# Kernel optimization log

Hardware: AMD Instinct MI355X
Metric: run time of the kernel (lower is better)

The kernel has to match this reference:

```python
import jax, jax.numpy as jnp
import numpy as np

N_NODES = 100000
N_EDGES = 3200000
IN_F, HID, OUT_F = 128, 3, 4


def setup_inputs() -> dict:
    key = jax.random.key(0)
    k1, k2, k3, k4, k5, k6 = jax.random.split(key, 6)
    x = jax.random.normal(k1, (N_NODES, IN_F), dtype=jnp.float32)
    edge_index = jax.random.randint(k2, (2, N_EDGES), 0, N_NODES, dtype=jnp.int64)
    # GCNConv weight (glorot) + bias, Linear(3,4) weight + bias
    W = jax.random.normal(k3, (IN_F, HID), dtype=jnp.float32) * (1.0 / np.sqrt(IN_F))
    b = jnp.zeros((HID,), dtype=jnp.float32)
    Wout = jax.random.normal(k4, (HID, OUT_F), dtype=jnp.float32) * (1.0 / np.sqrt(HID))
    bout = jax.random.normal(k5, (OUT_F,), dtype=jnp.float32) * 0.01
    return {"x": x, "edge_index": edge_index, "W": W, "b": b, "Wout": Wout, "bout": bout}


def reference(x, edge_index, W, b, Wout, bout):
    N = x.shape[0]
    # add self loops (PyG GCNConv default: add_self_loops=True)
    loop = jnp.arange(N, dtype=edge_index.dtype)
    row = jnp.concatenate([edge_index[0], loop])  # source nodes
    col = jnp.concatenate([edge_index[1], loop])  # destination nodes
    # linear transform first (cheaper: 128 -> 3)
    xw = x @ W  # [N, 3]
    # symmetric degree normalization: deg computed on destination index
    deg = jax.ops.segment_sum(jnp.ones_like(col, dtype=x.dtype), col, num_segments=N)
    dinv = jnp.where(deg > 0, jax.lax.rsqrt(deg), 0.0)
    norm = dinv[row] * dinv[col]  # [E+N]
    # gather source features, scale, scatter-add to destinations
    msg = xw[row] * norm[:, None]  # [E+N, 3]
    agg = jax.ops.segment_sum(msg, col, num_segments=N)  # [N, 3]
    h = jax.nn.relu(agg + b)
    z = h @ Wout + bout
    return (h, z)
```

## Files before the change

kernel.cpp:

```cpp
#include <hip/hip_runtime.h>
#include <hip/hip_fp16.h>

#define N_NODES 100000
#define N_EDGES 3200000
#define IN_F    128
#define HID     3
#define OUT_F   4

#define DSH     10
#define DTILE   1024
#define DMASK   1023
#define NSTRIPE 98
#define SSH     12
#define STILE   4096
#define SMASK   4095
#define NTILE   25
#define NCH     16

#define NBLKA   1024
#define THRA    256
#define EPB     ((N_EDGES + NBLKA - 1) / NBLKA)
#define N1      (NSTRIPE * NBLKA)

#define SCAN_ITEMS 16
#define SCAN_BLOCK 256
#define SCAN_PER_BLOCK (SCAN_ITEMS * SCAN_BLOCK)
#define NS1 ((N1 + SCAN_PER_BLOCK - 1) / SCAN_PER_BLOCK)

#define PSZ (NSTRIPE * DTILE * 3)

typedef float f32x4 __attribute__((ext_vector_type(4)));

__global__ void xw_kernel(const float* __restrict__ x,
                          const float* __restrict__ W,
                          float* __restrict__ xw) {
    int wave = threadIdx.x >> 6;
    int lane = threadIdx.x & 63;
    int half = lane >> 5;
    int l    = lane & 31;
    int node = blockIdx.x * 8 + wave * 2 + half;
    if (node >= N_NODES) return;
    f32x4 xv = __builtin_nontemporal_load(
        reinterpret_cast<const f32x4*>(x + (size_t)node * IN_F + l * 4));
    const float* w = W + l * 4 * HID;
    float s0 = xv.x * w[0] + xv.y * w[3] + xv.z * w[6] + xv.w * w[9];
    float s1 = xv.x * w[1] + xv.y * w[4] + xv.z * w[7] + xv.w * w[10];
    float s2 = xv.x * w[2] + xv.y * w[5] + xv.z * w[8] + xv.w * w[11];
    #pragma unroll
    for (int off = 16; off > 0; off >>= 1) {
        s0 += __shfl_down(s0, off, 32);
        s1 += __shfl_down(s1, off, 32);
        s2 += __shfl_down(s2, off, 32);
    }
    if (l == 0) {
        xw[node * 3 + 0] = s0;
        xw[node * 3 + 1] = s1;
        xw[node * 3 + 2] = s2;
    }
}

__global__ __launch_bounds__(THRA) void hist1_kernel(const int* __restrict__ col,
                                                     int* __restrict__ histG) {
    __shared__ int hist[8 * NSTRIPE];
    int tid = threadIdx.x, blk = blockIdx.x;
    for (int i = tid; i < 8 * NSTRIPE; i += THRA) hist[i] = 0;
    __syncthreads();
    int start = blk * EPB, end = min(start + EPB, N_EDGES);
    for (int e = start + tid; e < end; e += THRA)
        atomicAdd(&hist[(tid & 7) * NSTRIPE +
                        (__builtin_nontemporal_load(&col[e]) >> DSH)], 1);
    __syncthreads();
    for (int s = tid; s < NSTRIPE; s += THRA) {
        int v = 0;
        #pragma unroll
        for (int r = 0; r < 8; ++r) v += hist[r * NSTRIPE + s];
        histG[s * NBLKA + blk] = v;
    }
}

__global__ void scan1_kernel(int* __restrict__ data, int* __restrict__ bsum) {
    __shared__ int s[SCAN_BLOCK];
    int tid = threadIdx.x;
    int base = blockIdx.x * SCAN_PER_BLOCK + tid * SCAN_ITEMS;
    int v[SCAN_ITEMS];
    int tsum = 0;
    #pragma unroll
    for (int j = 0; j < SCAN_ITEMS; ++j) {
        v[j] = (base + j < N1) ? data[base + j] : 0;
        tsum += v[j];
    }
    s[tid] = tsum;
    __syncthreads();
    for (int off = 1; off < SCAN_BLOCK; off <<= 1) {
        int t = (tid >= off) ? s[tid - off] : 0;
        __syncthreads();
        s[tid] += t;
        __syncthreads();
    }
    int run = s[tid] - tsum;
    #pragma unroll
    for (int j = 0; j < SCAN_ITEMS; ++j) {
        int t = v[j];
        if (base + j < N1) data[base + j] = run;
        run += t;
    }
    if (tid == SCAN_BLOCK - 1) bsum[blockIdx.x] = s[SCAN_BLOCK - 1];
}

__global__ void scan2_kernel(int* __restrict__ bsum) {
    __shared__ int s[SCAN_BLOCK];
    int tid = threadIdx.x;
    int v = (tid < NS1) ? bsum[tid] : 0;
    s[tid] = v;
    __syncthreads();
    for (int off = 1; off < SCAN_BLOCK; off <<= 1) {
        int t = (tid >= off) ? s[tid - off] : 0;
        __syncthreads();
        s[tid] += t;
        __syncthreads();
    }
    if (tid < NS1) bsum[tid] = s[tid] - v;
}

__global__ void scan3_kernel(int* __restrict__ data, const int* __restrict__ bsum) {
    int i = blockIdx.x * blockDim.x + threadIdx.x;
    if (i < N1) data[i] += bsum[i / SCAN_PER_BLOCK];
}

__global__ __launch_bounds__(THRA) void fill1_kernel(const int* __restrict__ row,
                                                     const int* __restrict__ col,
                                                     const int* __restrict__ histG,
                                                     int* __restrict__ packed1) {
    __shared__ int offs[NSTRIPE];
    int tid = threadIdx.x, blk = blockIdx.x;
    for (int i = tid; i < NSTRIPE; i += THRA) offs[i] = histG[i * NBLKA + blk];
    __syncthreads();
    int start = blk * EPB, end = min(start + EPB, N_EDGES);
    for (int e = start + tid; e < end; e += THRA) {
        int c = __builtin_nontemporal_load(&col[e]);
        int r = __builtin_nontemporal_load(&row[e]);
        int s = c >> DSH;
        int pos = atomicAdd(&offs[s], 1);
        packed1[pos] = (r << DSH) | (c & DMASK);
    }
}

__global__ __launch_bounds__(1024) void prep_kernel(const int* __restrict__ histG,
                                                    const int* __restrict__ packed1,
                                                    const float* __restrict__ xw,
                                                    uint2* __restrict__ tab,
                                                    int* __restrict__ off2) {
    __shared__ int cnt[DTILE];
    __shared__ int h2[NTILE * NCH];
    __shared__ int sc[NTILE * NCH];
    int tid = threadIdx.x, s = blockIdx.x;
    for (int i = tid; i < DTILE; i += 1024) cnt[i] = 0;
    if (tid < NTILE * NCH) h2[tid] = 0;
    __syncthreads();
    int seg0 = histG[s * NBLKA];
    int seg1 = (s + 1 < NSTRIPE) ? histG[(s + 1) * NBLKA] : N_EDGES;
    int seglen = seg1 - seg0;
    int chsz = (seglen + NCH - 1) / NCH;
    if (chsz == 0) chsz = 1;
    for (int i = seg0 + tid; i < seg1; i += 1024) {
        int p = __builtin_nontemporal_load(&packed1[i]);
        atomicAdd(&cnt[p & DMASK], 1);
        int t = p >> (DSH + SSH);
        int ch = (i - seg0) / chsz;
        atomicAdd(&h2[t * NCH + ch], 1);
    }
    __syncthreads();
    if (tid < NTILE * NCH) sc[tid] = h2[tid];
    __syncthreads();
    for (int off = 1; off < NTILE * NCH; off <<= 1) {
        int v = 0;
        if (tid < NTILE * NCH && tid >= off) v = sc[tid - off];
        __syncthreads();
        if (tid < NTILE * NCH) sc[tid] += v;
        __syncthreads();
    }
    if (tid < NTILE * NCH)
        off2[s * (NTILE * NCH) + tid] = seg0 + sc[tid] - h2[tid];
    if (tid < DTILE) {
        int node = s * DTILE + tid;
        if (node < N_NODES) {
            float d = rsqrtf((float)(cnt[tid] + 1));
            __half2 lo = __floats2half2_rn(xw[node * 3 + 0] * d, xw[node * 3 + 1] * d);
            __half2 hi = __floats2half2_rn(xw[node * 3 + 2] * d, d);
            uint2 u;
            u.x = *reinterpret_cast<unsigned int*>(&lo);
            u.y = *reinterpret_cast<unsigned int*>(&hi);
            tab[node] = u;
        }
    }
}

__global__ __launch_bounds__(256) void fill2_kernel(const int* __restrict__ histG,
                                                    const int* __restrict__ off2,
                                                    const int* __restrict__ packed1,
                                                    int* __restrict__ packed2) {
    __shared__ int offs[NTILE];
    int tid = threadIdx.x;
    int s = blockIdx.x >> 4;
    int c = blockIdx.x & (NCH - 1);
    int seg0 = histG[s * NBLKA];
    int seg1 = (s + 1 < NSTRIPE) ? histG[(s + 1) * NBLKA] : N_EDGES;
    int seglen = seg1 - seg0;
    int chsz = (seglen + NCH - 1) / NCH;
    if (chsz == 0) chsz = 1;
    if (tid < NTILE) offs[tid] = off2[s * (NTILE * NCH) + tid * NCH + c];
    __syncthreads();
    int lo = seg0 + c * chsz;
    int hi = min(lo + chsz, seg1);
    for (int i = lo + tid; i < hi; i += 256) {
        int p = __builtin_nontemporal_load(&packed1[i]);
        int t = p >> (DSH + SSH);
        int pos = atomicAdd(&offs[t], 1);
        packed2[pos] = (((p >> DSH) & SMASK) << DSH) | (p & DMASK);
    }
}

__global__ __launch_bounds__(512) void aggF_kernel(const int* __restrict__ histG,
                                                   const int* __restrict__ off2,
                                                   const int* __restrict__ packed2,
                                                   const uint2* __restrict__ tab,
                                                   float* __restrict__ partial) {
    __shared__ uint2 stab[STILE];
    __shared__ float acc[DTILE * 3];
    const int tq[5] = {0, 7, 13, 19, 25};
    int tid = threadIdx.x;
    int s = blockIdx.x >> 2;
    int q = blockIdx.x & 3;
    for (int i = tid; i < DTILE * 3; i += 512) acc[i] = 0.f;
    int seg1 = (s + 1 < NSTRIPE) ? histG[(s + 1) * NBLKA] : N_EDGES;
    for (int t = tq[q]; t < tq[q + 1]; ++t) {
        __syncthreads();
        for (int i = tid; i < STILE; i += 512) {
            int g = t * STILE + i;
            uint2 u = (g < N_NODES) ? tab[g] : make_uint2(0u, 0u);
            stab[i] = u;
        }
        __syncthreads();
        int b0 = off2[s * (NTILE * NCH) + t * NCH];
        int b1 = (t + 1 < NTILE) ? off2[s * (NTILE * NCH) + (t + 1) * NCH] : seg1;
        for (int i = b0 + tid; i < b1; i += 512) {
            int p = __builtin_nontemporal_load(&packed2[i]);
            uint2 v = stab[p >> DSH];
            __half2 lo = *reinterpret_cast<__half2*>(&v.x);
            __half2 hi = *reinterpret_cast<__half2*>(&v.y);
            float2 f0 = __half22float2(lo);
            float2 f1 = __half22float2(hi);
            int a = (p & DMASK) * 3;
            atomicAdd(&acc[a + 0], f0.x);
            atomicAdd(&acc[a + 1], f0.y);
            atomicAdd(&acc[a + 2], f1.x);
        }
    }
    __syncthreads();
    float* P = partial + (size_t)q * PSZ + (size_t)s * (DTILE * 3);
    for (int i = tid; i < DTILE * 3; i += 512) P[i] = acc[i];
}

__global__ __launch_bounds__(256) void final_kernel(const float* __restrict__ partial,
                                                    const uint2* __restrict__ tab,
                                                    const float* __restrict__ bb,
                                                    const float* __restrict__ Wout,
                                                    const float* __restrict__ bout,
                                                    float* __restrict__ out) {
    int i = blockIdx.x * 256 + threadIdx.x;
    if (i >= N_NODES) return;
    uint2 u = tab[i];
    __half2 lo = *reinterpret_cast<__half2*>(&u.x);
    __half2 hi = *reinterpret_cast<__half2*>(&u.y);
    float2 f0 = __half22float2(lo);
    float2 f1 = __half22float2(hi);
    float g0 = f0.x, g1 = f0.y, g2 = f1.x;
    float di = f1.y;
    #pragma unroll
    for (int q = 0; q < 4; ++q) {
        const float* P = partial + (size_t)q * PSZ + (size_t)i * 3;
        g0 += P[0];
        g1 += P[1];
        g2 += P[2];
    }
    float h0 = fmaxf(g0 * di + bb[0], 0.f);
    float h1 = fmaxf(g1 * di + bb[1], 0.f);
    float h2 = fmaxf(g2 * di + bb[2], 0.f);
    out[i * 3 + 0] = h0;
    out[i * 3 + 1] = h1;
    out[i * 3 + 2] = h2;
    float* z = out + (size_t)N_NODES * 3;
    #pragma unroll
    for (int k = 0; k < 4; ++k) {
        z[i * 4 + k] = bout[k] + h0 * Wout[0 * 4 + k] + h1 * Wout[1 * 4 + k]
                                 + h2 * Wout[2 * 4 + k];
    }
}

static inline size_t align256(size_t x) { return (x + 255) & ~(size_t)255; }

extern "C" void kernel_launch(void* const* d_in, const int* in_sizes, int n_in,
                              void* d_out, int out_size, void* d_ws, size_t ws_size,
                              hipStream_t stream) {
    const float* x    = (const float*)d_in[0];
    const int*   ei   = (const int*)d_in[1];
    const float* W    = (const float*)d_in[2];
    const float* b    = (const float*)d_in[3];
    const float* Wout = (const float*)d_in[4];
    const float* bout = (const float*)d_in[5];
    float* out = (float*)d_out;

    char* wsb = (char*)d_ws;
    size_t off = 0;
    int*   histG   = (int*)(wsb + off);  off = align256(off + (size_t)N1 * 4);
    int*   packed1 = (int*)(wsb + off);  off = align256(off + (size_t)N_EDGES * 4);
    int*   packed2 = (int*)(wsb + off);  off = align256(off + (size_t)N_EDGES * 4);
    float* xw      = (float*)(wsb + off); off = align256(off + (size_t)N_NODES * 3 * 4);
    uint2* tab     = (uint2*)(wsb + off); off = align256(off + (size_t)N_NODES * 8);
    int*   off2    = (int*)(wsb + off);  off = align256(off + (size_t)NSTRIPE * NTILE * NCH * 4);
    float* partial = (float*)(wsb + off); off = align256(off + (size_t)4 * PSZ * 4);
    int*   bsum    = (int*)(wsb + off);  off = align256(off + (size_t)NS1 * 4);

    const int* row = ei;
    const int* col = ei + N_EDGES;

    xw_kernel<<<(N_NODES + 7) / 8, 256, 0, stream>>>(x, W, xw);
    hist1_kernel<<<NBLKA, THRA, 0, stream>>>(col, histG);
    scan1_kernel<<<NS1, SCAN_BLOCK, 0, stream>>>(histG, bsum);
    scan2_kernel<<<1, SCAN_BLOCK, 0, stream>>>(bsum);
    scan3_kernel<<<(N1 + 255) / 256, 256, 0, stream>>>(histG, bsum);
    fill1_kernel<<<NBLKA, THRA, 0, stream>>>(row, col, histG, packed1);
    prep_kernel<<<NSTRIPE, 1024, 0, stream>>>(histG, packed1, xw, tab, off2);
    fill2_kernel<<<NSTRIPE * NCH, 256, 0, stream>>>(histG, off2, packed1, packed2);
    aggF_kernel<<<NSTRIPE * 4, 512, 0, stream>>>(histG, off2, packed2, tab, partial);
    final_kernel<<<(N_NODES + 255) / 256, 256, 0, stream>>>(partial, tab, b, Wout, bout, out);
}
```

Baseline: 282.4 us.

## Replace two-level bucketing with per-stripe LDS radix sort and CSR gather-reduce

Shrinks destination stripes to 256 nodes and radix-sorts each stripe's packed edges in shared memory by local destination id, producing CSR offsets and sorted source lists. A new gather kernel sums source features per destination with four threads each and fuses ReLU and the output linear layer. This removes the second fill pass, the LDS float atomics, the 4-way partial buffers and the final combine kernel. It risks silently dropping edges if a stripe exceeds the fixed shared-memory capacity, and the sort's heavy LDS use limits occupancy.

```diff
diff --git a/kernel.cpp b/kernel.cpp
--- a/kernel.cpp
+++ b/kernel.cpp
@@ -7,15 +7,12 @@
 #define HID     3
 #define OUT_F   4
 
-#define DSH     10
-#define DTILE   1024
-#define DMASK   1023
-#define NSTRIPE 98
-#define SSH     12
-#define STILE   4096
-#define SMASK   4095
-#define NTILE   25
-#define NCH     16
+#define DBITS   8
+#define DTILE   256
+#define DMASK   255
+#define NSTRIPE 391
+#define MAXE    12288
+#define MAXIT   24
 
 #define NBLKA   1024
 #define THRA    256
@@ -26,8 +23,6 @@
 #define SCAN_BLOCK 256
 #define SCAN_PER_BLOCK (SCAN_ITEMS * SCAN_BLOCK)
 #define NS1 ((N1 + SCAN_PER_BLOCK - 1) / SCAN_PER_BLOCK)
-
-#define PSZ (NSTRIPE * DTILE * 3)
 
 typedef float f32x4 __attribute__((ext_vector_type(4)));
 
@@ -68,7 +63,7 @@
     int start = blk * EPB, end = min(start + EPB, N_EDGES);
     for (int e = start + tid; e < end; e += THRA)
         atomicAdd(&hist[(tid & 7) * NSTRIPE +
-                        (__builtin_nontemporal_load(&col[e]) >> DSH)], 1);
+                        (__builtin_nontemporal_load(&col[e]) >> DBITS)], 1);
     __syncthreads();
     for (int s = tid; s < NSTRIPE; s += THRA) {
         int v = 0;
@@ -139,161 +134,166 @@
     for (int e = start + tid; e < end; e += THRA) {
         int c = __builtin_nontemporal_load(&col[e]);
         int r = __builtin_nontemporal_load(&row[e]);
-        int s = c >> DSH;
+        int s = c >> DBITS;
         int pos = atomicAdd(&offs[s], 1);
-        packed1[pos] = (r << DSH) | (c & DMASK);
-    }
-}
-
-__global__ __launch_bounds__(1024) void prep_kernel(const int* __restrict__ histG,
-                                                    const int* __restrict__ packed1,
-                                                    const float* __restrict__ xw,
-                                                    uint2* __restrict__ tab,
-                                                    int* __restrict__ off2) {
-    __shared__ int cnt[DTILE];
-    __shared__ int h2[NTILE * NCH];
-    __shared__ int sc[NTILE * NCH];
+        packed1[pos] = (r << DBITS) | (c & DMASK);
+    }
+}
+
+__global__ __launch_bounds__(512, 1) void sortA_kernel(const int* __restrict__ histG,
+                                                       const int* __restrict__ packed1,
+                                                       const float* __restrict__ xw,
+                                                       uint2* __restrict__ tab,
+                                                       int* __restrict__ csrOff,
+                                                       int* __restrict__ srcSorted) {
+    __shared__ int ping[MAXE];
+    __shared__ int pong[MAXE];
+    __shared__ int cntW[4 * MAXIT * 8];
+    __shared__ int bounds[DTILE + 1];
     int tid = threadIdx.x, s = blockIdx.x;
-    for (int i = tid; i < DTILE; i += 1024) cnt[i] = 0;
-    if (tid < NTILE * NCH) h2[tid] = 0;
-    __syncthreads();
+    int lane = tid & 63, wv = tid >> 6;
+    unsigned long long ltmask = (lane == 63) ? ~0ULL >> 1
+                                             : (1ULL << lane) - 1;
+
     int seg0 = histG[s * NBLKA];
     int seg1 = (s + 1 < NSTRIPE) ? histG[(s + 1) * NBLKA] : N_EDGES;
-    int seglen = seg1 - seg0;
-    int chsz = (seglen + NCH - 1) / NCH;
-    if (chsz == 0) chsz = 1;
-    for (int i = seg0 + tid; i < seg1; i += 1024) {
-        int p = __builtin_nontemporal_load(&packed1[i]);
-        atomicAdd(&cnt[p & DMASK], 1);
-        int t = p >> (DSH + SSH);
-        int ch = (i - seg0) / chsz;
-        atomicAdd(&h2[t * NCH + ch], 1);
-    }
-    __syncthreads();
-    if (tid < NTILE * NCH) sc[tid] = h2[tid];
-    __syncthreads();
-    for (int off = 1; off < NTILE * NCH; off <<= 1) {
-        int v = 0;
-        if (tid < NTILE * NCH && tid >= off) v = sc[tid - off];
-        __syncthreads();
-        if (tid < NTILE * NCH) sc[tid] += v;
-        __syncthreads();
-    }
-    if (tid < NTILE * NCH)
-        off2[s * (NTILE * NCH) + tid] = seg0 + sc[tid] - h2[tid];
+    int len = min(seg1 - seg0, MAXE);
+    int nIter = (len + 511) >> 9;
+
+    for (int i = tid; i < len; i += 512)
+        ping[i] = __builtin_nontemporal_load(&packed1[seg0 + i]);
+    __syncthreads();
+
+    int* srcb = ping;
+    int* dstb = pong;
+    for (int shift = 0; shift < DBITS; shift += 2) {
+        for (int it = 0; it < nIter; ++it) {
+            int idx = it * 512 + tid;
+            int bk = (idx < len) ? ((srcb[idx] >> shift) & 3) : -1;
+            unsigned long long m0 = __ballot(bk == 0);
+            unsigned long long m1 = __ballot(bk == 1);
+            unsigned long long m2 = __ballot(bk == 2);
+            unsigned long long m3 = __ballot(bk == 3);
+            if (lane == 0) {
+                cntW[(0 * nIter + it) * 8 + wv] = __popcll(m0);
+                cntW[(1 * nIter + it) * 8 + wv] = __popcll(m1);
+                cntW[(2 * nIter + it) * 8 + wv] = __popcll(m2);
+                cntW[(3 * nIter + it) * 8 + wv] = __popcll(m3);
+            }
+        }
+        __syncthreads();
+        if (wv == 0) {
+            int n = 4 * nIter * 8;
+            int carry = 0;
+            int nch = (n + 63) >> 6;
+            for (int c = 0; c < nch; ++c) {
+                int i = c * 64 + lane;
+                int v = (i < n) ? cntW[i] : 0;
+                int x = v;
+                #pragma unroll
+                for (int o = 1; o < 64; o <<= 1) {
+                    int t = __shfl_up(x, o, 64);
+                    if (lane >= o) x += t;
+                }
+                if (i < n) cntW[i] = carry + x - v;
+                carry += __shfl(x, 63, 64);
+            }
+        }
+        __syncthreads();
+        for (int it = 0; it < nIter; ++it) {
+            int idx = it * 512 + tid;
+            int p = (idx < len) ? srcb[idx] : 0;
+            int bk = (idx < len) ? ((p >> shift) & 3) : -1;
+            unsigned long long m0 = __ballot(bk == 0);
+            unsigned long long m1 = __ballot(bk == 1);
+            unsigned long long m2 = __ballot(bk == 2);
+            unsigned long long m3 = __ballot(bk == 3);
+            if (idx < len) {
+                unsigned long long mk = (bk == 0) ? m0 : (bk == 1) ? m1
+                                      : (bk == 2) ? m2 : m3;
+                int base = cntW[(bk * nIter + it) * 8 + wv];
+                int rank = __popcll(mk & ltmask);
+                dstb[base + rank] = p;
+            }
+        }
+        __syncthreads();
+        int* t = srcb; srcb = dstb; dstb = t;
+    }
+    if (tid <= DTILE) {
+        int target = tid;
+        int lo = 0, hi = len;
+        while (lo < hi) {
+            int mid = (lo + hi) >> 1;
+            if ((ping[mid] & DMASK) < target) lo = mid + 1; else hi = mid;
+        }
+        bounds[tid] = lo;
+    }
+    __syncthreads();
+    int nodeBase = s * DTILE;
+    if (tid <= DTILE) {
+        int node = nodeBase + tid;
+        if (node <= N_NODES) csrOff[node] = seg0 + bounds[tid];
+    }
     if (tid < DTILE) {
-        int node = s * DTILE + tid;
+        int node = nodeBase + tid;
         if (node < N_NODES) {
-            float d = rsqrtf((float)(cnt[tid] + 1));
-            __half2 lo = __floats2half2_rn(xw[node * 3 + 0] * d, xw[node * 3 + 1] * d);
-            __half2 hi = __floats2half2_rn(xw[node * 3 + 2] * d, d);
+            int deg = bounds[tid + 1] - bounds[tid];
+            float d = rsqrtf((float)(deg + 1));
+            __half2 lo2 = __floats2half2_rn(xw[node * 3 + 0] * d, xw[node * 3 + 1] * d);
+            __half2 hi2 = __floats2half2_rn(xw[node * 3 + 2] * d, d);
             uint2 u;
-            u.x = *reinterpret_cast<unsigned int*>(&lo);
-            u.y = *reinterpret_cast<unsigned int*>(&hi);
+            u.x = *reinterpret_cast<unsigned int*>(&lo2);
+            u.y = *reinterpret_cast<unsigned int*>(&hi2);
             tab[node] = u;
         }
     }
-}
-
-__global__ __launch_bounds__(256) void fill2_kernel(const int* __restrict__ histG,
-                                                    const int* __restrict__ off2,
-                                                    const int* __restrict__ packed1,
-                                                    int* __restrict__ packed2) {
-    __shared__ int offs[NTILE];
-    int tid = threadIdx.x;
-    int s = blockIdx.x >> 4;
-    int c = blockIdx.x & (NCH - 1);
-    int seg0 = histG[s * NBLKA];
-    int seg1 = (s + 1 < NSTRIPE) ? histG[(s + 1) * NBLKA] : N_EDGES;
-    int seglen = seg1 - seg0;
-    int chsz = (seglen + NCH - 1) / NCH;
-    if (chsz == 0) chsz = 1;
-    if (tid < NTILE) offs[tid] = off2[s * (NTILE * NCH) + tid * NCH + c];
-    __syncthreads();
-    int lo = seg0 + c * chsz;
-    int hi = min(lo + chsz, seg1);
-    for (int i = lo + tid; i < hi; i += 256) {
-        int p = __builtin_nontemporal_load(&packed1[i]);
-        int t = p >> (DSH + SSH);
-        int pos = atomicAdd(&offs[t], 1);
-        packed2[pos] = (((p >> DSH) & SMASK) << DSH) | (p & DMASK);
-    }
-}
-
-__global__ __launch_bounds__(512) void aggF_kernel(const int* __restrict__ histG,
-                                                   const int* __restrict__ off2,
-                                                   const int* __restrict__ packed2,
-                                                   const uint2* __restrict__ tab,
-                                                   float* __restrict__ partial) {
-    __shared__ uint2 stab[STILE];
-    __shared__ float acc[DTILE * 3];
-    const int tq[5] = {0, 7, 13, 19, 25};
-    int tid = threadIdx.x;
-    int s = blockIdx.x >> 2;
-    int q = blockIdx.x & 3;
-    for (int i = tid; i < DTILE * 3; i += 512) acc[i] = 0.f;
-    int seg1 = (s + 1 < NSTRIPE) ? histG[(s + 1) * NBLKA] : N_EDGES;
-    for (int t = tq[q]; t < tq[q + 1]; ++t) {
-        __syncthreads();
-        for (int i = tid; i < STILE; i += 512) {
-            int g = t * STILE + i;
-            uint2 u = (g < N_NODES) ? tab[g] : make_uint2(0u, 0u);
-            stab[i] = u;
-        }
-        __syncthreads();
-        int b0 = off2[s * (NTILE * NCH) + t * NCH];
-        int b1 = (t + 1 < NTILE) ? off2[s * (NTILE * NCH) + (t + 1) * NCH] : seg1;
-        for (int i = b0 + tid; i < b1; i += 512) {
-            int p = __builtin_nontemporal_load(&packed2[i]);
-            uint2 v = stab[p >> DSH];
-            __half2 lo = *reinterpret_cast<__half2*>(&v.x);
-            __half2 hi = *reinterpret_cast<__half2*>(&v.y);
-            float2 f0 = __half22float2(lo);
-            float2 f1 = __half22float2(hi);
-            int a = (p & DMASK) * 3;
-            atomicAdd(&acc[a + 0], f0.x);
-            atomicAdd(&acc[a + 1], f0.y);
-            atomicAdd(&acc[a + 2], f1.x);
-        }
-    }
-    __syncthreads();
-    float* P = partial + (size_t)q * PSZ + (size_t)s * (DTILE * 3);
-    for (int i = tid; i < DTILE * 3; i += 512) P[i] = acc[i];
-}
-
-__global__ __launch_bounds__(256) void final_kernel(const float* __restrict__ partial,
-                                                    const uint2* __restrict__ tab,
-                                                    const float* __restrict__ bb,
-                                                    const float* __restrict__ Wout,
-                                                    const float* __restrict__ bout,
-                                                    float* __restrict__ out) {
-    int i = blockIdx.x * 256 + threadIdx.x;
-    if (i >= N_NODES) return;
-    uint2 u = tab[i];
-    __half2 lo = *reinterpret_cast<__half2*>(&u.x);
-    __half2 hi = *reinterpret_cast<__half2*>(&u.y);
-    float2 f0 = __half22float2(lo);
-    float2 f1 = __half22float2(hi);
-    float g0 = f0.x, g1 = f0.y, g2 = f1.x;
-    float di = f1.y;
-    #pragma unroll
-    for (int q = 0; q < 4; ++q) {
-        const float* P = partial + (size_t)q * PSZ + (size_t)i * 3;
-        g0 += P[0];
-        g1 += P[1];
-        g2 += P[2];
-    }
-    float h0 = fmaxf(g0 * di + bb[0], 0.f);
-    float h1 = fmaxf(g1 * di + bb[1], 0.f);
-    float h2 = fmaxf(g2 * di + bb[2], 0.f);
-    out[i * 3 + 0] = h0;
-    out[i * 3 + 1] = h1;
-    out[i * 3 + 2] = h2;
-    float* z = out + (size_t)N_NODES * 3;
-    #pragma unroll
-    for (int k = 0; k < 4; ++k) {
-        z[i * 4 + k] = bout[k] + h0 * Wout[0 * 4 + k] + h1 * Wout[1 * 4 + k]
-                                 + h2 * Wout[2 * 4 + k];
+    for (int i = tid; i < len; i += 512)
+        srcSorted[seg0 + i] = ping[i] >> DBITS;
+}
+
+__global__ __launch_bounds__(512) void reduceB_kernel(const int* __restrict__ csrOff,
+                                                      const int* __restrict__ srcSorted,
+                                                      const uint2* __restrict__ tab,
+                                                      const float* __restrict__ bb,
+                                                      const float* __restrict__ Wout,
+                                                      const float* __restrict__ bout,
+                                                      float* __restrict__ out) {
+    int gid = blockIdx.x * 512 + threadIdx.x;
+    int dest = gid >> 2, sub = gid & 3;
+    if (dest >= N_NODES) return;
+    int start = csrOff[dest], end = csrOff[dest + 1];
+    float a0 = 0.f, a1 = 0.f, a2 = 0.f;
+    for (int i = start + sub; i < end; i += 4) {
+        int r = srcSorted[i];
+        uint2 u = tab[r];
+        __half2 lo = *reinterpret_cast<__half2*>(&u.x);
+        __half2 hi = *reinterpret_cast<__half2*>(&u.y);
+        float2 f0 = __half22float2(lo);
+        float2 f1 = __half22float2(hi);
+        a0 += f0.x; a1 += f0.y; a2 += f1.x;
+    }
+    a0 += __shfl_down(a0, 2, 64); a1 += __shfl_down(a1, 2, 64); a2 += __shfl_down(a2, 2, 64);
+    a0 += __shfl_down(a0, 1, 64); a1 += __shfl_down(a1, 1, 64); a2 += __shfl_down(a2, 1, 64);
+    if (sub == 0) {
+        uint2 u = tab[dest];
+        __half2 lo = *reinterpret_cast<__half2*>(&u.x);
+        __half2 hi = *reinterpret_cast<__half2*>(&u.y);
+        float2 f0 = __half22float2(lo);
+        float2 f1 = __half22float2(hi);
+        float di = f1.y;
+        float h0 = fmaxf((a0 + f0.x) * di + bb[0], 0.f);
+        float h1 = fmaxf((a1 + f0.y) * di + bb[1], 0.f);
+        float h2 = fmaxf((a2 + f1.x) * di + bb[2], 0.f);
+        out[dest * 3 + 0] = h0;
+        out[dest * 3 + 1] = h1;
+        out[dest * 3 + 2] = h2;
+        float* z = out + (size_t)N_NODES * 3;
+        #pragma unroll
+        for (int k = 0; k < 4; ++k) {
+            z[dest * 4 + k] = bout[k] + h0 * Wout[0 * 4 + k]
+                                      + h1 * Wout[1 * 4 + k]
+                                      + h2 * Wout[2 * 4 + k];
+        }
     }
 }
 
@@ -312,14 +312,13 @@
 
     char* wsb = (char*)d_ws;
     size_t off = 0;
-    int*   histG   = (int*)(wsb + off);  off = align256(off + (size_t)N1 * 4);
-    int*   packed1 = (int*)(wsb + off);  off = align256(off + (size_t)N_EDGES * 4);
-    int*   packed2 = (int*)(wsb + off);  off = align256(off + (size_t)N_EDGES * 4);
-    float* xw      = (float*)(wsb + off); off = align256(off + (size_t)N_NODES * 3 * 4);
-    uint2* tab     = (uint2*)(wsb + off); off = align256(off + (size_t)N_NODES * 8);
-    int*   off2    = (int*)(wsb + off);  off = align256(off + (size_t)NSTRIPE * NTILE * NCH * 4);
-    float* partial = (float*)(wsb + off); off = align256(off + (size_t)4 * PSZ * 4);
-    int*   bsum    = (int*)(wsb + off);  off = align256(off + (size_t)NS1 * 4);
+    int*   histG     = (int*)(wsb + off);  off = align256(off + (size_t)N1 * 4);
+    int*   packed1   = (int*)(wsb + off);  off = align256(off + (size_t)N_EDGES * 4);
+    int*   srcSorted = (int*)(wsb + off);  off = align256(off + (size_t)N_EDGES * 4);
+    float* xw        = (float*)(wsb + off); off = align256(off + (size_t)N_NODES * 3 * 4);
+    uint2* tab       = (uint2*)(wsb + off); off = align256(off + (size_t)N_NODES * 8);
+    int*   csrOff    = (int*)(wsb + off);  off = align256(off + ((size_t)N_NODES + 1) * 4);
+    int*   bsum      = (int*)(wsb + off);  off = align256(off + (size_t)NS1 * 4);
 
     const int* row = ei;
     const int* col = ei + N_EDGES;
@@ -330,8 +329,7 @@
     scan2_kernel<<<1, SCAN_BLOCK, 0, stream>>>(bsum);
     scan3_kernel<<<(N1 + 255) / 256, 256, 0, stream>>>(histG, bsum);
     fill1_kernel<<<NBLKA, THRA, 0, stream>>>(row, col, histG, packed1);
-    prep_kernel<<<NSTRIPE, 1024, 0, stream>>>(histG, packed1, xw, tab, off2);
-    fill2_kernel<<<NSTRIPE * NCH, 256, 0, stream>>>(histG, off2, packed1, packed2);
-    aggF_kernel<<<NSTRIPE * 4, 512, 0, stream>>>(histG, off2, packed2, tab, partial);
-    final_kernel<<<(N_NODES + 255) / 256, 256, 0, stream>>>(partial, tab, b, Wout, bout, out);
-}
+    sortA_kernel<<<NSTRIPE, 512, 0, stream>>>(histG, packed1, xw, tab, csrOff, srcSorted);
+    reduceB_kernel<<<(N_NODES * 4 + 511) / 512, 512, 0, stream>>>(csrOff, srcSorted, tab,
+                                                                  b, Wout, bout, out);
+}
```

Measured after the change: 299.6 us. 6.1% more time.
